# Optimization experiments

Hardware: AMD Instinct MI355X
Metric: run time of the kernel (lower is better)

The kernel has to match this reference:

```python
import jax, jax.numpy as jnp
import numpy as np

FEAT_DIM = 128
GUIDE_DIM = 128
HIDDEN = [1024, 512, 256, 128]
OUT_DIM = 2


def make_coord(shape):
    # grid-center coords in (-1, 1), matching the torch make_coord
    seqs = [(-1.0 + 1.0 / n) + (2.0 / n) * jnp.arange(n, dtype=jnp.float32) for n in shape]
    yy, xx = jnp.meshgrid(seqs[0], seqs[1], indexing='ij')
    return jnp.stack([yy, xx], axis=-1)  # [h, w, 2]


def grid_sample_nearest(img, coord):
    # img: [B, C, H, W]; coord: [B, N, 2] with coord[...,0] along H, coord[...,1] along W
    # replicates F.grid_sample(img, coord.flip(-1)..., mode='nearest', align_corners=False,
    # padding_mode='zeros') followed by permute -> [B, N, C]
    B, C, H, W = img.shape
    iy = jnp.round(((coord[..., 0] + 1.0) * H - 1.0) * 0.5)
    ix = jnp.round(((coord[..., 1] + 1.0) * W - 1.0) * 0.5)
    valid = (iy >= 0) & (iy < H) & (ix >= 0) & (ix < W)
    iyc = jnp.clip(iy, 0, H - 1).astype(jnp.int32)
    ixc = jnp.clip(ix, 0, W - 1).astype(jnp.int32)
    g = jax.vmap(lambda im, y, x: im[:, y, x])(img, iyc, ixc)  # [B, C, N]
    g = g * valid[:, None, :].astype(img.dtype)  # zero padding outside
    return jnp.transpose(g, (0, 2, 1))  # [B, N, C]


def mlp(x, params):
    for W, b in params[:-1]:
        x = jax.nn.relu(x @ W + b)
    W, b = params[-1]
    return x @ W + b


def setup_inputs() -> dict:
    key = jax.random.key(0)
    ks = jax.random.split(key, 16)
    B, h, w = 4, 64, 64
    H_hr = W_hr = 256
    N = H_hr * W_hr  # 65536 query points
    feat = jax.random.normal(ks[0], (B, FEAT_DIM, h, w), jnp.float32)
    coord = jax.random.uniform(ks[1], (B, N, 2), jnp.float32, minval=-1.0, maxval=1.0)
    hr_guide = jax.random.normal(ks[2], (B, GUIDE_DIM, H_hr, W_hr), jnp.float32)
    lr_guide = jax.random.normal(ks[3], (B, GUIDE_DIM, h, w), jnp.float32)
    in_dim = FEAT_DIM + 2 * GUIDE_DIM + 2  # 386
    dims = [in_dim] + HIDDEN + [OUT_DIM]
    inp = {"feat": feat, "coord": coord, "hr_guide": hr_guide, "lr_guide": lr_guide}
    for i in range(len(dims) - 1):
        scale = 1.0 / np.sqrt(dims[i]).astype(np.float32)
        inp[f"W{i}"] = jax.random.normal(ks[4 + 2 * i], (dims[i], dims[i + 1]), jnp.float32) * scale
        inp[f"b{i}"] = jnp.zeros((dims[i + 1],), jnp.float32)
    return inp


def reference(feat, coord, hr_guide, lr_guide, W0, b0, W1, b1, W2, b2, W3, b3, W4, b4):
    params = [(W0, b0), (W1, b1), (W2, b2), (W3, b3), (W4, b4)]
    B, C, h, w = feat.shape
    N = coord.shape[1]
    fc = make_coord((h, w))  # [h, w, 2]
    feat_coord = jnp.broadcast_to(jnp.transpose(fc, (2, 0, 1))[None], (B, 2, h, w))
    q_guide_hr = grid_sample_nearest(hr_guide, coord)  # [B, N, G]
    rx = 1.0 / h
    ry = 1.0 / w
    hw = jnp.array([h, w], dtype=coord.dtype)
    preds = []
    for vx in (-1.0, 1.0):
        for vy in (-1.0, 1.0):
            shift = jnp.array([vx * rx, vy * ry], dtype=coord.dtype)
            coord_ = coord + shift
            q_feat = grid_sample_nearest(feat, coord_)        # [B, N, C]
            q_coord = grid_sample_nearest(feat_coord, coord_)  # [B, N, 2]
            rel_coord = (coord - q_coord) * hw                 # [B, N, 2]
            q_guide_lr = grid_sample_nearest(lr_guide, coord_)  # [B, N, G]
            inp = jnp.concatenate([q_feat, q_guide_hr, q_guide_hr - q_guide_lr, rel_coord], axis=-1)
            pred = mlp(inp.reshape(B * N, -1), params).reshape(B, N, OUT_DIM)
            preds.append(pred)
    preds = jnp.stack(preds, axis=-1)  # [B, N, 2, 4]
    weight = jax.nn.softmax(preds[:, :, 1, :], axis=-1)  # [B, N, 4]
    ret = jnp.sum(preds[:, :, 0, :] * weight, axis=-1, keepdims=True)  # [B, N, 1]
    return ret
```

## Files before the change

### kernel.cpp

```cpp
#include <hip/hip_runtime.h>
#include <cstdint>
#include <cstddef>


typedef unsigned short u16;
typedef unsigned int u32;
typedef _Float16 half8 __attribute__((ext_vector_type(8)));
typedef float floatx4 __attribute__((ext_vector_type(4)));
typedef float floatx2 __attribute__((ext_vector_type(2)));
typedef u32 u32x2 __attribute__((ext_vector_type(2)));
typedef u32 u32x4 __attribute__((ext_vector_type(4)));

__device__ __forceinline__ u16 f2h(float x) {
    _Float16 h = (_Float16)x;
    return __builtin_bit_cast(unsigned short, h);
}
__device__ __forceinline__ float h2f(u16 u) {
    return (float)__builtin_bit_cast(_Float16, u);
}

__device__ __forceinline__ void cp_async16(const void* gsrc, void* lds) {
#if defined(__has_builtin) && __has_builtin(__builtin_amdgcn_global_load_lds)
    __builtin_amdgcn_global_load_lds(
        (__attribute__((address_space(1))) void*)(uintptr_t)gsrc,
        (__attribute__((address_space(3))) void*)(uint32_t)(uintptr_t)lds,
        16, 0, 0);
#else
    *(u32x4*)lds = *(const u32x4*)gsrc;
#endif
}

__global__ void transpose_chw_hwc(const float* __restrict__ src,
                                  u16* __restrict__ dst, int HW) {
    __shared__ float t[32][33];
    const int b = blockIdx.z;
    const int hw0 = blockIdx.x * 32, c0 = blockIdx.y * 32;
    const float* s = src + (size_t)b * 128 * HW;
    u16* d = dst + (size_t)b * HW * 128;
    const int tx = threadIdx.x, ty = threadIdx.y;
#pragma unroll
    for (int j = 0; j < 4; ++j)
        t[ty + j * 8][tx] = s[(size_t)(c0 + ty + j * 8) * HW + hw0 + tx];
    __syncthreads();
#pragma unroll
    for (int j = 0; j < 4; ++j)
        d[(size_t)(hw0 + ty + j * 8) * 128 + c0 + tx] = f2h(t[tx][ty + j * 8]);
}

__global__ void prep_wt(const float* __restrict__ W, u16* __restrict__ Wt,
                        int K, int N, int perm) {
    int idx = blockIdx.x * 256 + threadIdx.x;
    if (idx >= N * K) return;
    int nn = idx / K, kk = idx - nn * K;
    int ka = kk;
    if (perm) {
        int s = kk & 63;
        ka = (kk & ~63) + ((s & 3) << 4) + (s >> 2);
    }
    Wt[idx] = f2h(W[(size_t)ka * N + nn]);
}

__global__ __launch_bounds__(256) void gather_build(
    const float* __restrict__ coord, const u16* __restrict__ hrT,
    const u16* __restrict__ featT, const u16* __restrict__ lrT,
    u16* __restrict__ X, float* __restrict__ rel, int p0) {
    const int wid = threadIdx.x >> 6, lane = threadIdx.x & 63;
    const int pl = blockIdx.x * 4 + wid;
    const int p = p0 + pl;
    const int b = p >> 16;
    const float cy = coord[(size_t)p * 2];
    const float cx = coord[(size_t)p * 2 + 1];
    const u32* hr32 = (const u32*)hrT;
    const u32* ft32 = (const u32*)featT;
    const u32* lr32 = (const u32*)lrT;

    float fy = rintf(((cy + 1.0f) * 256.0f - 1.0f) * 0.5f);
    float fx = rintf(((cx + 1.0f) * 256.0f - 1.0f) * 0.5f);
    bool vh = (fy >= 0.0f) && (fy < 256.0f) && (fx >= 0.0f) && (fx < 256.0f);
    int iy = (int)fminf(fmaxf(fy, 0.0f), 255.0f);
    int ix = (int)fminf(fmaxf(fx, 0.0f), 255.0f);
    u32 hrv = hr32[((((size_t)b * 256 + iy) * 256 + ix) * 128 >> 1) + lane];
    if (!vh) hrv = 0u;
    const float hr_lo = h2f((u16)(hrv & 0xffffu));
    const float hr_hi = h2f((u16)(hrv >> 16));

    const size_t rowbase = (size_t)pl * 4;
#pragma unroll
    for (int s = 0; s < 4; ++s) {
        float sy = (s & 2) ? 0.015625f : -0.015625f;
        float sx = (s & 1) ? 0.015625f : -0.015625f;
        float gy = rintf(((cy + sy + 1.0f) * 64.0f - 1.0f) * 0.5f);
        float gx = rintf(((cx + sx + 1.0f) * 64.0f - 1.0f) * 0.5f);
        bool v = (gy >= 0.0f) && (gy < 64.0f) && (gx >= 0.0f) && (gx < 64.0f);
        int jy = (int)fminf(fmaxf(gy, 0.0f), 63.0f);
        int jx = (int)fminf(fmaxf(gx, 0.0f), 63.0f);
        size_t g32 = ((((size_t)b * 64 + jy) * 64 + jx) * 128 >> 1) + lane;
        u32 fv = ft32[g32];
        u32 lv = lr32[g32];
        if (!v) { fv = 0u; lv = 0u; }
        u16 d_lo = f2h(hr_lo - h2f((u16)(lv & 0xffffu)));
        u16 d_hi = f2h(hr_hi - h2f((u16)(lv >> 16)));

        u32* xr = (u32*)(X + (rowbase + s) * 384);
        xr[lane] = fv;
        xr[64 + lane] = hrv;
        xr[128 + lane] = (u32)d_lo | ((u32)d_hi << 16);

        if (lane == 0) {
            float qcy = v ? (-0.984375f + 0.03125f * (float)jy) : 0.0f;
            float qcx = v ? (-0.984375f + 0.03125f * (float)jx) : 0.0f;
            rel[(rowbase + s) * 2 + 0] = (cy - qcy) * 64.0f;
            rel[(rowbase + s) * 2 + 1] = (cx - qcx) * 64.0f;
        }
    }
}

__global__ __launch_bounds__(512, 2) void gemm_f16_256(
    const u16* __restrict__ A, const u16* __restrict__ Bt,
    const float* __restrict__ bias, u16* __restrict__ C, int K, int N,
    int lognb, const float* __restrict__ rel, const float* __restrict__ w0tail) {
    __shared__ __align__(16) u16 sA[2][2][8192];
    __shared__ __align__(16) u16 sB[2][2][8192];
    const int tid = threadIdx.x;
    const int lane = tid & 63;
    const int wid = tid >> 6;
    const int r = lane & 15, q = lane >> 4;
    const int wm = wid >> 2, wn = wid & 3;

    const int g = blockIdx.x;
    const int n_idx = (g >> 3) & ((1 << lognb) - 1);
    const int m_idx = (g & 7) + ((g >> (3 + lognb)) << 3);
    const int n0 = n_idx << 8;
    const u32 m0 = (u32)m_idx << 8;

    const u32 srow = (u32)(tid >> 2);
    const u32 gchunk = (u32)((tid & 3) ^ ((tid >> 3) & 3));
    const u32 gaoff = (m0 + srow) * (u32)K + (gchunk << 3);
    const u32 gboff = ((u32)n0 + srow) * (u32)K + (gchunk << 3);

    auto stageA = [&](int kt, int ks, int buf) {
        const u16* gp = A + gaoff + (u32)((kt << 6) + (ks << 5));
        u16* lp = &sA[buf][ks][tid << 3];
        cp_async16(gp, lp);
        cp_async16(gp + ((u32)K << 7), lp + 4096);
    };
    auto stageB = [&](int kt, int ks, int buf) {
        const u16* gp = Bt + gboff + (u32)((kt << 6) + (ks << 5));
        u16* lp = &sB[buf][ks][tid << 3];
        cp_async16(gp, lp);
        cp_async16(gp + ((u32)K << 7), lp + 4096);
    };

    const int fs = (q ^ ((r >> 1) & 3)) << 3;
    const int abase = ((wm << 7) + r) * 32 + fs;
    const int bbase = ((wn << 6) + r) * 32 + fs;

    floatx4 acc[8][4];
#pragma unroll
    for (int mi = 0; mi < 8; ++mi)
#pragma unroll
        for (int ni = 0; ni < 4; ++ni)
            acc[mi][ni] = (floatx4){0.0f, 0.0f, 0.0f, 0.0f};

    const int nk = K >> 6;
    stageA(0, 0, 0);
    stageA(0, 1, 0);
    stageB(0, 0, 0);
    stageB(0, 1, 0);
    const int k1 = (nk > 1) ? 1 : 0;
    stageA(k1, 0, 1);
    stageA(k1, 1, 1);
    stageB(k1, 1, 1);
    asm volatile("s_waitcnt vmcnt(6)");
    __builtin_amdgcn_s_barrier();

    for (int kt = 0; kt < nk; ++kt) {
        const int cur = kt & 1, nxt = cur ^ 1;
        const bool p1 = (kt + 1) < nk;
        const bool p2 = (kt + 2) < nk;
        half8 a0[8], a1[8], bf[2];
#pragma unroll
        for (int mi = 0; mi < 8; ++mi)
            a0[mi] = *(const half8*)&sA[cur][0][abase + (mi << 9)];
#pragma unroll
        for (int ni = 0; ni < 2; ++ni)
            bf[ni] = *(const half8*)&sB[cur][0][bbase + (ni << 9)];
        if (p1) stageB(kt + 1, 0, nxt);
        __builtin_amdgcn_s_barrier();
        asm volatile("s_waitcnt lgkmcnt(0)");
        __builtin_amdgcn_s_setprio(1);
#pragma unroll
        for (int mi = 0; mi < 8; ++mi)
#pragma unroll
            for (int ni = 0; ni < 2; ++ni)
                acc[mi][ni] = __builtin_amdgcn_mfma_f32_16x16x32_f16(
                    a0[mi], bf[ni], acc[mi][ni], 0, 0, 0);
        __builtin_amdgcn_s_setprio(0);
        __builtin_amdgcn_s_barrier();
#pragma unroll
        for (int mi = 0; mi < 8; ++mi)
            a1[mi] = *(const half8*)&sA[cur][1][abase + (mi << 9)];
#pragma unroll
        for (int ni = 0; ni < 2; ++ni)
            bf[ni] = *(const half8*)&sB[cur][1][bbase + (ni << 9)];
        if (p2) stageA(kt + 2, 0, cur);
        __builtin_amdgcn_s_barrier();
        asm volatile("s_waitcnt lgkmcnt(0)");
        __builtin_amdgcn_s_setprio(1);
#pragma unroll
        for (int mi = 0; mi < 8; ++mi)
#pragma unroll
            for (int ni = 0; ni < 2; ++ni)
                acc[mi][ni] = __builtin_amdgcn_mfma_f32_16x16x32_f16(
                    a1[mi], bf[ni], acc[mi][ni], 0, 0, 0);
        __builtin_amdgcn_s_setprio(0);
        __builtin_amdgcn_s_barrier();
#pragma unroll
        for (int ni = 0; ni < 2; ++ni)
            bf[ni] = *(const half8*)&sB[cur][1][bbase + 1024 + (ni << 9)];
        if (p2) stageA(kt + 2, 1, cur);
        __builtin_amdgcn_s_barrier();
        asm volatile("s_waitcnt lgkmcnt(0)");
        __builtin_amdgcn_s_setprio(1);
#pragma unroll
        for (int mi = 0; mi < 8; ++mi)
#pragma unroll
            for (int ni = 0; ni < 2; ++ni)
                acc[mi][2 + ni] = __builtin_amdgcn_mfma_f32_16x16x32_f16(
                    a1[mi], bf[ni], acc[mi][2 + ni], 0, 0, 0);
        __builtin_amdgcn_s_setprio(0);
        __builtin_amdgcn_s_barrier();
#pragma unroll
        for (int ni = 0; ni < 2; ++ni)
            bf[ni] = *(const half8*)&sB[cur][0][bbase + 1024 + (ni << 9)];
        if (p2) stageB(kt + 2, 1, cur);
        __builtin_amdgcn_s_barrier();
        asm volatile("s_waitcnt lgkmcnt(0)");
        __builtin_amdgcn_s_setprio(1);
#pragma unroll
        for (int mi = 0; mi < 8; ++mi)
#pragma unroll
            for (int ni = 0; ni < 2; ++ni)
                acc[mi][2 + ni] = __builtin_amdgcn_mfma_f32_16x16x32_f16(
                    a0[mi], bf[ni], acc[mi][2 + ni], 0, 0, 0);
        __builtin_amdgcn_s_setprio(0);
        if (p2) {
            asm volatile("s_waitcnt vmcnt(6)");
        } else {
            asm volatile("s_waitcnt vmcnt(0)");
        }
        __builtin_amdgcn_s_barrier();
    }

    float bias_v[4], w0a[4], w0b[4];
#pragma unroll
    for (int nig = 0; nig < 4; ++nig) {
        int col = n0 + (wn << 6) + nig * 16 + r;
        bias_v[nig] = bias[col];
        w0a[nig] = rel ? w0tail[col] : 0.0f;
        w0b[nig] = rel ? w0tail[N + col] : 0.0f;
    }
#pragma unroll
    for (int mi = 0; mi < 8; ++mi) {
#pragma unroll
        for (int rr = 0; rr < 4; ++rr) {
            u32 row = m0 + (u32)(wm << 7) + (u32)(mi << 4) + (u32)(q << 2) +
                      (u32)rr;
            float rl0 = 0.0f, rl1 = 0.0f;
            if (rel) {
                floatx2 rl = *(const floatx2*)&rel[(size_t)row * 2];
                rl0 = rl[0];
                rl1 = rl[1];
            }
            u32 pk[2];
#pragma unroll
            for (int h = 0; h < 2; ++h) {
                u32 w = 0;
#pragma unroll
                for (int j = 0; j < 2; ++j) {
                    int nig = h * 2 + j;
                    float v = acc[mi][nig][rr] + bias_v[nig];
                    if (rel) v += rl0 * w0a[nig] + rl1 * w0b[nig];
                    v = fmaxf(v, 0.0f);
                    w |= (u32)f2h(v) << (16 * j);
                }
                pk[h] = w;
            }
            *(u32x2*)(C + row * (u32)N + (u32)(n0 + (wn << 6) + (r << 2))) =
                (u32x2){pk[0], pk[1]};
        }
    }
}

__global__ __launch_bounds__(256, 3) void gemm_f16(
    const u16* __restrict__ A, const u16* __restrict__ Bt,
    const float* __restrict__ bias, u16* __restrict__ C, int K, int N,
    int lognb, const float* __restrict__ rel, const float* __restrict__ w0tail) {
    __shared__ __align__(16) u16 As[2][128 * 64];
    __shared__ __align__(16) u16 Bs[128 * 64];
    const int tid = threadIdx.x;
    const int lane = tid & 63;
    const int wid = tid >> 6;
    const int r = lane & 15, q = lane >> 4;
    const int wm = (wid & 1) << 6, wn = (wid >> 1) << 6;

    const int g = blockIdx.x;
    const int n_idx = (g >> 3) & ((1 << lognb) - 1);
    const int m_idx = (g & 7) + ((g >> (3 + lognb)) << 3);
    const int n0 = n_idx << 7;
    const u32 m0 = (u32)m_idx << 7;

    const int srow = tid >> 3;
    const int schunk = (tid & 7) ^ (srow & 7);
    const u32 gaoff = (m0 + (u32)srow) * (u32)K + ((u32)schunk << 3);
    const u32 gboff = (u32)(n0 + srow) * (u32)K + ((u32)schunk << 3);

    auto stageA = [&](int kt, int buf) {
        const u16* gak = A + gaoff + (kt << 6);
        u16* la = &As[buf][tid * 8];
#pragma unroll
        for (int i = 0; i < 4; ++i)
            cp_async16(gak + (u32)(i << 5) * (u32)K, la + (i << 11));
    };

    u32x4 breg[4];
    auto loadB = [&](int kt) {
        const u16* gbk = Bt + gboff + (kt << 6);
#pragma unroll
        for (int i = 0; i < 4; ++i)
            breg[i] = *(const u32x4*)(gbk + (u32)(i << 5) * (u32)K);
    };
    auto writeB = [&]() {
        u16* lb = &Bs[tid * 8];
#pragma unroll
        for (int i = 0; i < 4; ++i)
            *(u32x4*)(lb + (i << 11)) = breg[i];
    };

    const int cx = (q ^ (r & 7)) << 3;
    const int arow = (wm + r) << 6, brow = (wn + r) << 6;

    floatx4 acc[4][4];
#pragma unroll
    for (int mi = 0; mi < 4; ++mi)
#pragma unroll
        for (int ni = 0; ni < 4; ++ni)
            acc[mi][ni] = (floatx4){0.0f, 0.0f, 0.0f, 0.0f};

    const int nk = K >> 6;
    loadB(0);
    stageA(0, 0);
    writeB();
    __syncthreads();

    for (int kt = 0; kt < nk; ++kt) {
        const int cur = kt & 1;
        const bool pf = (kt + 1 < nk);
        if (pf) {
            loadB(kt + 1);
            stageA(kt + 1, cur ^ 1);
        }
#pragma unroll
        for (int ks = 0; ks < 2; ++ks) {
            half8 af[4], bfr[4];
#pragma unroll
            for (int mi = 0; mi < 4; ++mi)
                af[mi] = *(const half8*)&As[cur][arow + (mi << 10) + (cx ^ (ks << 5))];
#pragma unroll
            for (int ni = 0; ni < 4; ++ni)
                bfr[ni] = *(const half8*)&Bs[brow + (ni << 10) + (cx ^ (ks << 5))];
#pragma unroll
            for (int mi = 0; mi < 4; ++mi)
#pragma unroll
                for (int ni = 0; ni < 4; ++ni)
                    acc[mi][ni] = __builtin_amdgcn_mfma_f32_16x16x32_f16(
                        af[mi], bfr[ni], acc[mi][ni], 0, 0, 0);
        }
        if (pf) {
            __syncthreads();
            writeB();
            __syncthreads();
        }
    }

    float bias_v[4], w0a[4], w0b[4];
#pragma unroll
    for (int ni = 0; ni < 4; ++ni) {
        int col = n0 + wn + ni * 16 + r;
        bias_v[ni] = bias[col];
        w0a[ni] = rel ? w0tail[col] : 0.0f;
        w0b[ni] = rel ? w0tail[N + col] : 0.0f;
    }
#pragma unroll
    for (int mi = 0; mi < 4; ++mi) {
#pragma unroll
        for (int rr = 0; rr < 4; ++rr) {
            u32 row = m0 + wm + mi * 16 + q * 4 + rr;
            float rl0 = 0.0f, rl1 = 0.0f;
            if (rel) {
                floatx2 rl = *(const floatx2*)&rel[(size_t)row * 2];
                rl0 = rl[0];
                rl1 = rl[1];
            }
            u32 pk[2];
#pragma unroll
            for (int h = 0; h < 2; ++h) {
                u32 w = 0;
#pragma unroll
                for (int j = 0; j < 2; ++j) {
                    int ni = h * 2 + j;
                    float v = acc[mi][ni][rr] + bias_v[ni];
                    if (rel) v += rl0 * w0a[ni] + rl1 * w0b[ni];
                    v = fmaxf(v, 0.0f);
                    w |= (u32)f2h(v) << (16 * j);
                }
                pk[h] = w;
            }
            *(u32x2*)(C + row * (u32)N + (u32)(n0 + wn + (r << 2))) =
                (u32x2){pk[0], pk[1]};
        }
    }
}

__global__ __launch_bounds__(256) void l4_combine(
    const u16* __restrict__ A3, const float* __restrict__ W4,
    const float* __restrict__ b4, float* __restrict__ out, int p0) {
    const int wid = threadIdx.x >> 6, lane = threadIdx.x & 63;
    const int pl = blockIdx.x * 4 + wid;
    const int p2 = lane * 2;
    const int s0 = p2 & 63, bb = p2 & ~63;
    const int k0 = bb + ((s0 & 3) << 4) + (s0 >> 2);
    const int s1 = s0 + 1;
    const int k1 = bb + ((s1 & 3) << 4) + (s1 >> 2);
    const float w00 = W4[k0 * 2], w01 = W4[k0 * 2 + 1];
    const float w10 = W4[k1 * 2], w11 = W4[k1 * 2 + 1];
    float P0[4], P1[4];
#pragma unroll
    for (int s = 0; s < 4; ++s) {
        size_t rowoff = ((size_t)pl * 4 + s) * 128 + p2;
        u32 av = *(const u32*)(A3 + rowoff);
        float a0 = h2f((u16)(av & 0xffffu));
        float a1 = h2f((u16)(av >> 16));
        float d0 = a0 * w00 + a1 * w10;
        float d1 = a0 * w01 + a1 * w11;
#pragma unroll
        for (int m = 32; m >= 1; m >>= 1) {
            d0 += __shfl_xor(d0, m, 64);
            d1 += __shfl_xor(d1, m, 64);
        }
        P0[s] = d0 + b4[0];
        P1[s] = d1 + b4[1];
    }
    if (lane == 0) {
        float mx = fmaxf(fmaxf(P1[0], P1[1]), fmaxf(P1[2], P1[3]));
        float e0 = __expf(P1[0] - mx), e1 = __expf(P1[1] - mx);
        float e2 = __expf(P1[2] - mx), e3 = __expf(P1[3] - mx);
        float se = e0 + e1 + e2 + e3;
        out[p0 + pl] = (P0[0] * e0 + P0[1] * e1 + P0[2] * e2 + P0[3] * e3) / se;
    }
}

extern "C" void kernel_launch(void* const* d_in, const int* in_sizes, int n_in,
                              void* d_out, int out_size, void* d_ws,
                              size_t ws_size, hipStream_t stream) {
    const float* feat = (const float*)d_in[0];
    const float* coord = (const float*)d_in[1];
    const float* hr = (const float*)d_in[2];
    const float* lr = (const float*)d_in[3];
    const float* W0 = (const float*)d_in[4];
    const float* b0 = (const float*)d_in[5];
    const float* W1 = (const float*)d_in[6];
    const float* b1 = (const float*)d_in[7];
    const float* W2 = (const float*)d_in[8];
    const float* b2 = (const float*)d_in[9];
    const float* W3 = (const float*)d_in[10];
    const float* b3 = (const float*)d_in[11];
    const float* W4 = (const float*)d_in[12];
    const float* b4 = (const float*)d_in[13];
    float* out = (float*)d_out;

    char* base = (char*)d_ws;
    size_t off = 0;
    auto carve = [&](size_t bytes) -> char* {
        char* p = base + off;
        off += (bytes + 255) & ~(size_t)255;
        return p;
    };

    u16* hrT = (u16*)carve(4ull * 65536 * 128 * 2);
    u16* featT = (u16*)carve(4ull * 4096 * 128 * 2);
    u16* lrT = (u16*)carve(4ull * 4096 * 128 * 2);
    u16* Wt0 = (u16*)carve(1024ull * 384 * 2);
    u16* Wt1 = (u16*)carve(512ull * 1024 * 2);
    u16* Wt2 = (u16*)carve(256ull * 512 * 2);
    u16* Wt3 = (u16*)carve(128ull * 256 * 2);
    const size_t fixed = off;

    const size_t R = 1048576ull;
    int c = 16;
    for (; c < 8192; c *= 2) {
        size_t Rc = R / c;
        size_t need = fixed;
        size_t sizes[3] = {Rc * 1024, Rc * 8, Rc * 2048};
        for (int i = 0; i < 3; ++i) need += (sizes[i] + 255) & ~(size_t)255;
        if (need <= ws_size) break;
    }
    const size_t Rc = R / c;
    const int Pc = (int)(262144 / c);

    char* R1 = carve(Rc * 1024);
    float* rel = (float*)carve(Rc * 8);
    char* R2 = carve(Rc * 2048);
    u16* X = (u16*)R1;
    u16* A1 = (u16*)R1;
    u16* A0 = (u16*)R2;
    u16* A2 = (u16*)R2;
    u16* A3 = (u16*)(R2 + Rc * 512);

    transpose_chw_hwc<<<dim3(2048, 4, 4), dim3(32, 8), 0, stream>>>(hr, hrT, 65536);
    transpose_chw_hwc<<<dim3(128, 4, 4), dim3(32, 8), 0, stream>>>(feat, featT, 4096);
    transpose_chw_hwc<<<dim3(128, 4, 4), dim3(32, 8), 0, stream>>>(lr, lrT, 4096);
    prep_wt<<<(1024 * 384 + 255) / 256, 256, 0, stream>>>(W0, Wt0, 384, 1024, 0);
    prep_wt<<<(512 * 1024 + 255) / 256, 256, 0, stream>>>(W1, Wt1, 1024, 512, 1);
    prep_wt<<<(256 * 512 + 255) / 256, 256, 0, stream>>>(W2, Wt2, 512, 256, 1);
    prep_wt<<<(128 * 256 + 255) / 256, 256, 0, stream>>>(W3, Wt3, 256, 128, 1);

    const int mt1 = (int)(Rc / 128);
    const int mt2 = (int)(Rc / 256);
    const bool use256 = (Rc % 2048ull) == 0;
    for (int ci = 0; ci < c; ++ci) {
        const int p0 = ci * Pc;
        gather_build<<<Pc / 4, 256, 0, stream>>>(coord, hrT, featT, lrT, X, rel, p0);
        if (use256) {
            gemm_f16_256<<<mt2 * 4, 512, 0, stream>>>(X, Wt0, b0, A0, 384, 1024,
                                                      2, rel, W0 + 384 * 1024);
            gemm_f16_256<<<mt2 * 2, 512, 0, stream>>>(A0, Wt1, b1, A1, 1024, 512,
                                                      1, nullptr, nullptr);
            gemm_f16_256<<<mt2 * 1, 512, 0, stream>>>(A1, Wt2, b2, A2, 512, 256,
                                                      0, nullptr, nullptr);
        } else {
            gemm_f16<<<mt1 * 8, 256, 0, stream>>>(X, Wt0, b0, A0, 384, 1024, 3,
                                                  rel, W0 + 384 * 1024);
            gemm_f16<<<mt1 * 4, 256, 0, stream>>>(A0, Wt1, b1, A1, 1024, 512, 2,
                                                  nullptr, nullptr);
            gemm_f16<<<mt1 * 2, 256, 0, stream>>>(A1, Wt2, b2, A2, 512, 256, 1,
                                                  nullptr, nullptr);
        }
        gemm_f16<<<mt1 * 1, 256, 0, stream>>>(A2, Wt3, b3, A3, 256, 128, 0,
                                              nullptr, nullptr);
        l4_combine<<<Pc / 4, 256, 0, stream>>>(A3, W4, b4, out, p0);
    }
}
```

Baseline: 3.760 ms.

## Make 256-tile GEMM blocks loop over all N tiles with continuous prefetch

Each block of the 256x256 f16 GEMM now owns one M tile and walks through every N tile itself, instead of launching one block per (M,N) tile. The double-buffered cp_async pipeline runs across tile boundaries, so the next tile's B and A loads are issued before the current tile's epilogue. This removes the pipeline fill and drain per output tile and cuts block launch overhead. The cost is far fewer blocks in the grid, which can hurt load balance and tail behaviour. The A row tile is also re-streamed per N tile rather than shared across neighbouring blocks in L2.

```diff
diff --git a/kernel.cpp b/kernel.cpp
--- a/kernel.cpp
+++ b/kernel.cpp
@@ -118,7 +118,7 @@
 __global__ __launch_bounds__(512, 2) void gemm_f16_256(
     const u16* __restrict__ A, const u16* __restrict__ Bt,
     const float* __restrict__ bias, u16* __restrict__ C, int K, int N,
-    int lognb, const float* __restrict__ rel, const float* __restrict__ w0tail) {
+    int nt, const float* __restrict__ rel, const float* __restrict__ w0tail) {
     __shared__ __align__(16) u16 sA[2][2][8192];
     __shared__ __align__(16) u16 sB[2][2][8192];
     const int tid = threadIdx.x;
@@ -127,16 +127,12 @@
     const int r = lane & 15, q = lane >> 4;
     const int wm = wid >> 2, wn = wid & 3;
 
-    const int g = blockIdx.x;
-    const int n_idx = (g >> 3) & ((1 << lognb) - 1);
-    const int m_idx = (g & 7) + ((g >> (3 + lognb)) << 3);
-    const int n0 = n_idx << 8;
-    const u32 m0 = (u32)m_idx << 8;
+    const u32 m0 = (u32)blockIdx.x << 8;
 
     const u32 srow = (u32)(tid >> 2);
     const u32 gchunk = (u32)((tid & 3) ^ ((tid >> 3) & 3));
     const u32 gaoff = (m0 + srow) * (u32)K + (gchunk << 3);
-    const u32 gboff = ((u32)n0 + srow) * (u32)K + (gchunk << 3);
+    const u32 gboff0 = srow * (u32)K + (gchunk << 3);
 
     auto stageA = [&](int kt, int ks, int buf) {
         const u16* gp = A + gaoff + (u32)((kt << 6) + (ks << 5));
@@ -144,8 +140,9 @@
         cp_async16(gp, lp);
         cp_async16(gp + ((u32)K << 7), lp + 4096);
     };
-    auto stageB = [&](int kt, int ks, int buf) {
-        const u16* gp = Bt + gboff + (u32)((kt << 6) + (ks << 5));
+    auto stageB = [&](int tb, int kt, int ks, int buf) {
+        const u16* gp = Bt + gboff0 + (u32)(tb << 8) * (u32)K +
+                        (u32)((kt << 6) + (ks << 5));
         u16* lp = &sB[buf][ks][tid << 3];
         cp_async16(gp, lp);
         cp_async16(gp + ((u32)K << 7), lp + 4096);
@@ -163,132 +160,146 @@
             acc[mi][ni] = (floatx4){0.0f, 0.0f, 0.0f, 0.0f};
 
     const int nk = K >> 6;
+    const int total = nt * nk;
     stageA(0, 0, 0);
     stageA(0, 1, 0);
-    stageB(0, 0, 0);
-    stageB(0, 1, 0);
-    const int k1 = (nk > 1) ? 1 : 0;
-    stageA(k1, 0, 1);
-    stageA(k1, 1, 1);
-    stageB(k1, 1, 1);
+    stageB(0, 0, 0, 0);
+    stageB(0, 0, 1, 0);
+    stageA(1, 0, 1);
+    stageA(1, 1, 1);
+    stageB(0, 1, 1, 1);
     asm volatile("s_waitcnt vmcnt(6)");
     __builtin_amdgcn_s_barrier();
 
-    for (int kt = 0; kt < nk; ++kt) {
-        const int cur = kt & 1, nxt = cur ^ 1;
-        const bool p1 = (kt + 1) < nk;
-        const bool p2 = (kt + 2) < nk;
-        half8 a0[8], a1[8], bf[2];
+    for (int t = 0; t < nt; ++t) {
+        for (int kt = 0; kt < nk; ++kt) {
+            const int cur = kt & 1, nxt = cur ^ 1;
+            const int g = t * nk + kt;
+            const bool h1 = (g + 1) < total;
+            const bool h2 = (g + 2) < total;
+            const int in1 = (kt + 1) < nk;
+            const int tb1 = in1 ? t : t + 1;
+            const int kt1 = in1 ? kt + 1 : 0;
+            int kt2 = kt + 2, tb2 = t;
+            if (kt2 >= nk) { kt2 -= nk; tb2 = t + 1; }
+            half8 a0[8], a1[8], bf[2];
+#pragma unroll
+            for (int mi = 0; mi < 8; ++mi)
+                a0[mi] = *(const half8*)&sA[cur][0][abase + (mi << 9)];
+#pragma unroll
+            for (int ni = 0; ni < 2; ++ni)
+                bf[ni] = *(const half8*)&sB[cur][0][bbase + (ni << 9)];
+            if (h1) stageB(tb1, kt1, 0, nxt);
+            __builtin_amdgcn_s_barrier();
+            asm volatile("s_waitcnt lgkmcnt(0)");
+            __builtin_amdgcn_s_setprio(1);
+#pragma unroll
+            for (int mi = 0; mi < 8; ++mi)
+#pragma unroll
+                for (int ni = 0; ni < 2; ++ni)
+                    acc[mi][ni] = __builtin_amdgcn_mfma_f32_16x16x32_f16(
+                        a0[mi], bf[ni], acc[mi][ni], 0, 0, 0);
+            __builtin_amdgcn_s_setprio(0);
+            __builtin_amdgcn_s_barrier();
+#pragma unroll
+            for (int mi = 0; mi < 8; ++mi)
+                a1[mi] = *(const half8*)&sA[cur][1][abase + (mi << 9)];
+#pragma unroll
+            for (int ni = 0; ni < 2; ++ni)
+                bf[ni] = *(const half8*)&sB[cur][1][bbase + (ni << 9)];
+            if (h2) stageA(kt2, 0, cur);
+            __builtin_amdgcn_s_barrier();
+            asm volatile("s_waitcnt lgkmcnt(0)");
+            __builtin_amdgcn_s_setprio(1);
+#pragma unroll
+            for (int mi = 0; mi < 8; ++mi)
+#pragma unroll
+                for (int ni = 0; ni < 2; ++ni)
+                    acc[mi][ni] = __builtin_amdgcn_mfma_f32_16x16x32_f16(
+                        a1[mi], bf[ni], acc[mi][ni], 0, 0, 0);
+            __builtin_amdgcn_s_setprio(0);
+            __builtin_amdgcn_s_barrier();
+#pragma unroll
+            for (int ni = 0; ni < 2; ++ni)
+                bf[ni] = *(const half8*)&sB[cur][1][bbase + 1024 + (ni << 9)];
+            if (h2) stageA(kt2, 1, cur);
+            __builtin_amdgcn_s_barrier();
+            asm volatile("s_waitcnt lgkmcnt(0)");
+            __builtin_amdgcn_s_setprio(1);
+#pragma unroll
+            for (int mi = 0; mi < 8; ++mi)
+#pragma unroll
+                for (int ni = 0; ni < 2; ++ni)
+                    acc[mi][2 + ni] = __builtin_amdgcn_mfma_f32_16x16x32_f16(
+                        a1[mi], bf[ni], acc[mi][2 + ni], 0, 0, 0);
+            __builtin_amdgcn_s_setprio(0);
+            __builtin_amdgcn_s_barrier();
+#pragma unroll
+            for (int ni = 0; ni < 2; ++ni)
+                bf[ni] = *(const half8*)&sB[cur][0][bbase + 1024 + (ni << 9)];
+            if (h2) stageB(tb2, kt2, 1, cur);
+            __builtin_amdgcn_s_barrier();
+            asm volatile("s_waitcnt lgkmcnt(0)");
+            __builtin_amdgcn_s_setprio(1);
+#pragma unroll
+            for (int mi = 0; mi < 8; ++mi)
+#pragma unroll
+                for (int ni = 0; ni < 2; ++ni)
+                    acc[mi][2 + ni] = __builtin_amdgcn_mfma_f32_16x16x32_f16(
+                        a0[mi], bf[ni], acc[mi][2 + ni], 0, 0, 0);
+            __builtin_amdgcn_s_setprio(0);
+            if (h2) {
+                asm volatile("s_waitcnt vmcnt(6)");
+            } else {
+                asm volatile("s_waitcnt vmcnt(0)");
+            }
+            __builtin_amdgcn_s_barrier();
+        }
+
+        const int n0 = t << 8;
+        float bias_v[4], w0a[4], w0b[4];
+#pragma unroll
+        for (int nig = 0; nig < 4; ++nig) {
+            int col = n0 + (wn << 6) + nig * 16 + r;
+            bias_v[nig] = bias[col];
+            w0a[nig] = rel ? w0tail[col] : 0.0f;
+            w0b[nig] = rel ? w0tail[N + col] : 0.0f;
+        }
+#pragma unroll
+        for (int mi = 0; mi < 8; ++mi) {
+#pragma unroll
+            for (int rr = 0; rr < 4; ++rr) {
+                u32 row = m0 + (u32)(wm << 7) + (u32)(mi << 4) +
+                          (u32)(q << 2) + (u32)rr;
+                float rl0 = 0.0f, rl1 = 0.0f;
+                if (rel) {
+                    floatx2 rl = *(const floatx2*)&rel[(size_t)row * 2];
+                    rl0 = rl[0];
+                    rl1 = rl[1];
+                }
+                u32 pk[2];
+#pragma unroll
+                for (int h = 0; h < 2; ++h) {
+                    u32 w = 0;
+#pragma unroll
+                    for (int j = 0; j < 2; ++j) {
+                        int nig = h * 2 + j;
+                        float v = acc[mi][nig][rr] + bias_v[nig];
+                        if (rel) v += rl0 * w0a[nig] + rl1 * w0b[nig];
+                        v = fmaxf(v, 0.0f);
+                        w |= (u32)f2h(v) << (16 * j);
+                    }
+                    pk[h] = w;
+                }
+                *(u32x2*)(C + row * (u32)N + (u32)(n0 + (wn << 6) + (r << 2))) =
+                    (u32x2){pk[0], pk[1]};
+            }
+        }
 #pragma unroll
         for (int mi = 0; mi < 8; ++mi)
-            a0[mi] = *(const half8*)&sA[cur][0][abase + (mi << 9)];
-#pragma unroll
-        for (int ni = 0; ni < 2; ++ni)
-            bf[ni] = *(const half8*)&sB[cur][0][bbase + (ni << 9)];
-        if (p1) stageB(kt + 1, 0, nxt);
-        __builtin_amdgcn_s_barrier();
-        asm volatile("s_waitcnt lgkmcnt(0)");
-        __builtin_amdgcn_s_setprio(1);
-#pragma unroll
-        for (int mi = 0; mi < 8; ++mi)
-#pragma unroll
-            for (int ni = 0; ni < 2; ++ni)
-                acc[mi][ni] = __builtin_amdgcn_mfma_f32_16x16x32_f16(
-                    a0[mi], bf[ni], acc[mi][ni], 0, 0, 0);
-        __builtin_amdgcn_s_setprio(0);
-        __builtin_amdgcn_s_barrier();
-#pragma unroll
-        for (int mi = 0; mi < 8; ++mi)
-            a1[mi] = *(const half8*)&sA[cur][1][abase + (mi << 9)];
-#pragma unroll
-        for (int ni = 0; ni < 2; ++ni)
-            bf[ni] = *(const half8*)&sB[cur][1][bbase + (ni << 9)];
-        if (p2) stageA(kt + 2, 0, cur);
-        __builtin_amdgcn_s_barrier();
-        asm volatile("s_waitcnt lgkmcnt(0)");
-        __builtin_amdgcn_s_setprio(1);
-#pragma unroll
-        for (int mi = 0; mi < 8; ++mi)
-#pragma unroll
-            for (int ni = 0; ni < 2; ++ni)
-                acc[mi][ni] = __builtin_amdgcn_mfma_f32_16x16x32_f16(
-                    a1[mi], bf[ni], acc[mi][ni], 0, 0, 0);
-        __builtin_amdgcn_s_setprio(0);
-        __builtin_amdgcn_s_barrier();
-#pragma unroll
-        for (int ni = 0; ni < 2; ++ni)
-            bf[ni] = *(const half8*)&sB[cur][1][bbase + 1024 + (ni << 9)];
-        if (p2) stageA(kt + 2, 1, cur);
-        __builtin_amdgcn_s_barrier();
-        asm volatile("s_waitcnt lgkmcnt(0)");
-        __builtin_amdgcn_s_setprio(1);
-#pragma unroll
-        for (int mi = 0; mi < 8; ++mi)
-#pragma unroll
-            for (int ni = 0; ni < 2; ++ni)
-                acc[mi][2 + ni] = __builtin_amdgcn_mfma_f32_16x16x32_f16(
-                    a1[mi], bf[ni], acc[mi][2 + ni], 0, 0, 0);
-        __builtin_amdgcn_s_setprio(0);
-        __builtin_amdgcn_s_barrier();
-#pragma unroll
-        for (int ni = 0; ni < 2; ++ni)
-            bf[ni] = *(const half8*)&sB[cur][0][bbase + 1024 + (ni << 9)];
-        if (p2) stageB(kt + 2, 1, cur);
-        __builtin_amdgcn_s_barrier();
-        asm volatile("s_waitcnt lgkmcnt(0)");
-        __builtin_amdgcn_s_setprio(1);
-#pragma unroll
-        for (int mi = 0; mi < 8; ++mi)
-#pragma unroll
-            for (int ni = 0; ni < 2; ++ni)
-                acc[mi][2 + ni] = __builtin_amdgcn_mfma_f32_16x16x32_f16(
-                    a0[mi], bf[ni], acc[mi][2 + ni], 0, 0, 0);
-        __builtin_amdgcn_s_setprio(0);
-        if (p2) {
-            asm volatile("s_waitcnt vmcnt(6)");
-        } else {
-            asm volatile("s_waitcnt vmcnt(0)");
-        }
-        __builtin_amdgcn_s_barrier();
-    }
-
-    float bias_v[4], w0a[4], w0b[4];
-#pragma unroll
-    for (int nig = 0; nig < 4; ++nig) {
-        int col = n0 + (wn << 6) + nig * 16 + r;
-        bias_v[nig] = bias[col];
-        w0a[nig] = rel ? w0tail[col] : 0.0f;
-        w0b[nig] = rel ? w0tail[N + col] : 0.0f;
-    }
-#pragma unroll
-    for (int mi = 0; mi < 8; ++mi) {
-#pragma unroll
-        for (int rr = 0; rr < 4; ++rr) {
-            u32 row = m0 + (u32)(wm << 7) + (u32)(mi << 4) + (u32)(q << 2) +
-                      (u32)rr;
-            float rl0 = 0.0f, rl1 = 0.0f;
-            if (rel) {
-                floatx2 rl = *(const floatx2*)&rel[(size_t)row * 2];
-                rl0 = rl[0];
-                rl1 = rl[1];
-            }
-            u32 pk[2];
-#pragma unroll
-            for (int h = 0; h < 2; ++h) {
-                u32 w = 0;
-#pragma unroll
-                for (int j = 0; j < 2; ++j) {
-                    int nig = h * 2 + j;
-                    float v = acc[mi][nig][rr] + bias_v[nig];
-                    if (rel) v += rl0 * w0a[nig] + rl1 * w0b[nig];
-                    v = fmaxf(v, 0.0f);
-                    w |= (u32)f2h(v) << (16 * j);
-                }
-                pk[h] = w;
-            }
-            *(u32x2*)(C + row * (u32)N + (u32)(n0 + (wn << 6) + (r << 2))) =
-                (u32x2){pk[0], pk[1]};
-        }
+#pragma unroll
+            for (int ni = 0; ni < 4; ++ni)
+                acc[mi][ni] = (floatx4){0.0f, 0.0f, 0.0f, 0.0f};
     }
 }
 
@@ -532,12 +543,12 @@
         const int p0 = ci * Pc;
         gather_build<<<Pc / 4, 256, 0, stream>>>(coord, hrT, featT, lrT, X, rel, p0);
         if (use256) {
-            gemm_f16_256<<<mt2 * 4, 512, 0, stream>>>(X, Wt0, b0, A0, 384, 1024,
-                                                      2, rel, W0 + 384 * 1024);
-            gemm_f16_256<<<mt2 * 2, 512, 0, stream>>>(A0, Wt1, b1, A1, 1024, 512,
-                                                      1, nullptr, nullptr);
-            gemm_f16_256<<<mt2 * 1, 512, 0, stream>>>(A1, Wt2, b2, A2, 512, 256,
-                                                      0, nullptr, nullptr);
+            gemm_f16_256<<<mt2, 512, 0, stream>>>(X, Wt0, b0, A0, 384, 1024,
+                                                  4, rel, W0 + 384 * 1024);
+            gemm_f16_256<<<mt2, 512, 0, stream>>>(A0, Wt1, b1, A1, 1024, 512,
+                                                  2, nullptr, nullptr);
+            gemm_f16_256<<<mt2, 512, 0, stream>>>(A1, Wt2, b2, A2, 512, 256,
+                                                  1, nullptr, nullptr);
         } else {
             gemm_f16<<<mt1 * 8, 256, 0, stream>>>(X, Wt0, b0, A0, 384, 1024, 3,
                                                   rel, W0 + 384 * 1024);
```

Result: slower. 5.314 ms (+41.4%).
